# Kernel tuning notes

Measured on AMD Instinct MI355X. Metric: run time of the kernel, lower is better.

The kernel has to match this reference:

```python
import jax, jax.numpy as jnp
import numpy as np

E = 8          # num_configs
C = 256        # embed_dim
DIN = 4 * C    # embed_dim * (1 + 3 stat terms for max_order=2)
LN_EPS = 1e-5


def setup_inputs() -> dict:
    key = jax.random.key(0)
    ks = jax.random.split(key, 8)
    B, T = 4, 8192
    x = jax.random.normal(ks[0], (B, T, C), dtype=jnp.float32)
    mask = jax.random.randint(ks[1], (B, T), 0, 2, dtype=jnp.int32)
    ln_w = jnp.ones((C,), jnp.float32)
    ln_b = jnp.zeros((C,), jnp.float32)
    W1 = jax.random.normal(ks[2], (E, DIN, C), jnp.float32) / np.sqrt(DIN).astype(np.float32)
    b1 = jnp.zeros((E, C), jnp.float32)
    W2 = jax.random.normal(ks[3], (E, C, C), jnp.float32) / np.sqrt(C).astype(np.float32)
    b2 = jnp.zeros((E, C), jnp.float32)
    We = jax.random.normal(ks[4], (E, C), jnp.float32) / np.sqrt(C).astype(np.float32)
    be = jnp.zeros((E,), jnp.float32)
    log_beta = jnp.zeros((1,), jnp.float32)
    config_prior = jnp.zeros((E,), jnp.float32)
    return dict(x=x, mask=mask, ln_w=ln_w, ln_b=ln_b, W1=W1, b1=b1, W2=W2, b2=b2,
                We=We, be=be, log_beta=log_beta, config_prior=config_prior)


def _layernorm(x, w, b):
    mu = x.mean(axis=-1, keepdims=True)
    var = ((x - mu) ** 2).mean(axis=-1, keepdims=True)
    return (x - mu) * jax.lax.rsqrt(var + LN_EPS) * w + b


def reference(x, mask, ln_w, ln_b, W1, b1, W2, b2, We, be, log_beta, config_prior):
    B, T, Cd = x.shape
    m = mask.astype(bool)                         # [B,T]
    mf = m[..., None].astype(x.dtype)             # [B,T,1]

    h = _layernorm(x, ln_w, ln_b)                 # [B,T,C]

    # masked high-order statistics over T (max_order=2: mean, std, var)
    n = jnp.maximum(mf.sum(axis=1, keepdims=True), 1.0)          # [B,1,1]
    mean = (h * mf).sum(axis=1, keepdims=True) / n               # [B,1,C]
    var_b = (((h - mean) ** 2) * mf).sum(axis=1, keepdims=True) / n
    can = (n > 1.0).astype(x.dtype)
    corr = n / jnp.maximum(n - 1.0, 1e-9)
    var_u = var_b * corr * can + var_b * (1.0 - can)
    std_u = jnp.maximum(jnp.sqrt(var_u), 1e-9)

    bshape = (B, T, Cd)
    interaction = jnp.concatenate([
        x,
        jnp.broadcast_to(mean, bshape),
        jnp.broadcast_to(std_u, bshape),
        jnp.broadcast_to(var_u, bshape),
    ], axis=-1)                                                  # [B,T,4C]

    # ensemble of expert MLPs (batched over E)
    h1 = jax.nn.gelu(jnp.einsum('btd,edc->btec', interaction, W1) + b1, approximate=False)
    outputs = jnp.einsum('btec,ecf->btef', h1, W2) + b2          # [B,T,E,C]
    energies = jnp.einsum('btec,ec->bte', outputs, We) + be      # [B,T,E]

    # energy-weighted softmax mixture (partition function)
    beta = jnp.exp(log_beta)[0]
    neg_be = -beta * (energies + config_prior)                   # [B,T,E]
    big = jnp.finfo(x.dtype).max
    masked_nbe = jnp.where(m[..., None], neg_be, -big)
    log_Z = jax.nn.logsumexp(masked_nbe, axis=-1)                # [B,T]
    config_probs = jnp.exp(masked_nbe - log_Z[..., None]) * mf   # [B,T,E]

    out = jnp.einsum('bte,btec->btc', config_probs, outputs) * mf
    return out
```

## Files before the change

kernel.cpp:

```cpp
#include <hip/hip_runtime.h>
#include <cmath>

#define B_ 4
#define T_ 8192
#define C_ 256
#define E_ 8
#define M_ (B_*T_)

typedef __bf16 bf16x8 __attribute__((ext_vector_type(8)));
typedef float  f32x4  __attribute__((ext_vector_type(4)));

typedef const __attribute__((address_space(1))) unsigned int* gas_t;
typedef __attribute__((address_space(3))) unsigned int* las_t;

static __device__ __forceinline__ unsigned short f2bf(float f) {
    union { float fv; unsigned u; } v; v.fv = f;
    unsigned r = v.u + 0x7FFFu + ((v.u >> 16) & 1u);
    return (unsigned short)(r >> 16);
}

static __device__ __forceinline__ float fast_erf(float x) {
    float ax = fabsf(x);
    float t = __builtin_amdgcn_rcpf(1.0f + 0.3275911f * ax);
    float p = ((((1.061405429f * t - 1.453152027f) * t) + 1.421413741f) * t - 0.284496736f) * t + 0.254829592f;
    float y = 1.0f - p * t * __expf(-ax * ax);
    return copysignf(y, x);
}

static __device__ __forceinline__ float gelu_f(float x) {
    return 0.5f * x * (1.0f + fast_erf(x * 0.7071067811865476f));
}

static __device__ __forceinline__ f32x4 mfma16(bf16x8 a, bf16x8 b, f32x4 c) {
    return __builtin_amdgcn_mfma_f32_16x16x32_bf16(a, b, c, 0, 0, 0);
}

static __device__ __forceinline__ void stage_strip(const unsigned short* __restrict__ src,
                                                   unsigned short* base, int lane) {
#pragma unroll
    for (int j = 0; j < 8; j++) {
        int s = (j << 6) + lane;
        int col = s >> 3;
        int ks = (s & 7) ^ (col & 7);
        const unsigned short* gp = src + (col << 8) + (ks << 3);
        __builtin_amdgcn_global_load_lds((gas_t)(const void*)gp,
                                         (las_t)(void*)(base + (j << 9)), 16, 0, 0);
    }
}


__global__ void k_w1t(const float* __restrict__ W1, unsigned short* __restrict__ w1t) {
    __shared__ float tile[64][65];
    int e = blockIdx.x >> 4, kt = (blockIdx.x >> 2) & 3, ct = blockIdx.x & 3;
    int k0 = kt << 6, c0 = ct << 6;
    const float* src = W1 + ((size_t)e << 18) + ((size_t)k0 << 8) + c0;
    int r = threadIdx.x >> 6, col = threadIdx.x & 63;
#pragma unroll
    for (int i = 0; i < 16; i++)
        tile[r + i * 4][col] = src[(size_t)(r + i * 4) * 256 + col];
    __syncthreads();
    unsigned short* dst = w1t + (e << 16) + (c0 << 8) + k0;
#pragma unroll
    for (int i = 0; i < 16; i++)
        dst[(r + i * 4) * 256 + col] = f2bf(tile[col][r + i * 4]);
}

__global__ void k_w2t(const float* __restrict__ W2, unsigned short* __restrict__ w2t) {
    __shared__ float tile[64][65];
    int e = blockIdx.x >> 4, ct = (blockIdx.x >> 2) & 3, ft = blockIdx.x & 3;
    int c0 = ct << 6, f0 = ft << 6;
    const float* src = W2 + ((size_t)e << 16) + ((size_t)c0 << 8) + f0;
    int r = threadIdx.x >> 6, col = threadIdx.x & 63;
#pragma unroll
    for (int i = 0; i < 16; i++)
        tile[r + i * 4][col] = src[(size_t)(r + i * 4) * 256 + col];
    __syncthreads();
    unsigned short* dst = w2t + (e << 16) + (f0 << 8) + c0;
#pragma unroll
    for (int i = 0; i < 16; i++)
        dst[(r + i * 4) * 256 + col] = f2bf(tile[col][r + i * 4]);
}

__global__ void k_v2(const float* __restrict__ W2, const float* __restrict__ We,
                     const float* __restrict__ b2, const float* __restrict__ be,
                     const float* __restrict__ log_beta, const float* __restrict__ prior,
                     float* __restrict__ v2, float* __restrict__ bc2, float* __restrict__ bbeta) {
    __shared__ float sm[4];
    int e = blockIdx.x >> 8, c = blockIdx.x & 255, f = threadIdx.x;
    float wef = We[(e << 8) + f];
    float v = W2[((((e << 8) + c) << 8)) + f] * wef;
#pragma unroll
    for (int m = 32; m >= 1; m >>= 1) v += __shfl_xor(v, m);
    if ((f & 63) == 0) sm[f >> 6] = v;
    __syncthreads();
    if (f == 0) v2[(e << 8) + c] = sm[0] + sm[1] + sm[2] + sm[3];
    if (c == 0) {
        __syncthreads();
        float u = b2[(e << 8) + f] * wef;
#pragma unroll
        for (int m = 32; m >= 1; m >>= 1) u += __shfl_xor(u, m);
        if ((f & 63) == 0) sm[f >> 6] = u;
        __syncthreads();
        if (f == 0) {
            float beta = __expf(log_beta[0]);
            float c2e = sm[0] + sm[1] + sm[2] + sm[3] + be[e];
            bc2[e] = -beta * (c2e + prior[e]);
            if (e == 0) bbeta[0] = beta;
        }
    }
}

__global__ void k_stats(const float* __restrict__ x, const int* __restrict__ mask,
                        const float* __restrict__ lnw, const float* __restrict__ lnb,
                        float* __restrict__ S1, float* __restrict__ S2, float* __restrict__ ncnt,
                        unsigned short* __restrict__ xb) {
    int b = blockIdx.x >> 6;
    int chunk = blockIdx.x & 63;
    int wid = threadIdx.x >> 6, lane = threadIdx.x & 63;
    int c0 = lane << 2;
    float4 w4 = *reinterpret_cast<const float4*>(lnw + c0);
    float4 b4 = *reinterpret_cast<const float4*>(lnb + c0);
    float a1[4] = {0,0,0,0}, a2[4] = {0,0,0,0};
    int cnt = 0;
    int tbase = chunk * 128;
    for (int r = wid; r < 128; r += 4) {
        int row = b * T_ + tbase + r;
        float4 xv = *reinterpret_cast<const float4*>(x + (size_t)row * C_ + c0);
        ushort4 o;
        o.x = f2bf(xv.x); o.y = f2bf(xv.y); o.z = f2bf(xv.z); o.w = f2bf(xv.w);
        *reinterpret_cast<ushort4*>(xb + (size_t)row * C_ + c0) = o;
        float s1 = xv.x + xv.y + xv.z + xv.w;
        float s2 = xv.x*xv.x + xv.y*xv.y + xv.z*xv.z + xv.w*xv.w;
#pragma unroll
        for (int m = 1; m < 64; m <<= 1) { s1 += __shfl_xor(s1, m); s2 += __shfl_xor(s2, m); }
        if (mask[row]) {
            float mu = s1 * (1.f / C_);
            float var = s2 * (1.f / C_) - mu * mu;
            float rs = rsqrtf(var + 1e-5f);
            float hv;
            hv = (xv.x - mu) * rs * w4.x + b4.x; a1[0] += hv; a2[0] += hv * hv;
            hv = (xv.y - mu) * rs * w4.y + b4.y; a1[1] += hv; a2[1] += hv * hv;
            hv = (xv.z - mu) * rs * w4.z + b4.z; a1[2] += hv; a2[2] += hv * hv;
            hv = (xv.w - mu) * rs * w4.w + b4.w; a1[3] += hv; a2[3] += hv * hv;
            cnt++;
        }
    }
    __shared__ float red[4][256];
    __shared__ int rc[4];
#pragma unroll
    for (int j = 0; j < 4; j++) red[wid][c0 + j] = a1[j];
    if (lane == 0) rc[wid] = cnt;
    __syncthreads();
    int ch = threadIdx.x;
    float s = red[0][ch] + red[1][ch] + red[2][ch] + red[3][ch];
    atomicAdd(&S1[(b << 8) + ch], s);
    if (threadIdx.x == 0) atomicAdd(&ncnt[b], (float)(rc[0] + rc[1] + rc[2] + rc[3]));
    __syncthreads();
#pragma unroll
    for (int j = 0; j < 4; j++) red[wid][c0 + j] = a2[j];
    __syncthreads();
    s = red[0][ch] + red[1][ch] + red[2][ch] + red[3][ch];
    atomicAdd(&S2[(b << 8) + ch], s);
}

__global__ void k_stats_fin(const float* __restrict__ S1, const float* __restrict__ S2,
                            const float* __restrict__ ncnt, float* __restrict__ stats) {
    int b = blockIdx.x, c = threadIdx.x;
    float n = fmaxf(ncnt[b], 1.f);
    float mean = S1[(b << 8) + c] / n;
    float var_b = fmaxf(S2[(b << 8) + c] / n - mean * mean, 0.f);
    float var_u = (n > 1.f) ? (var_b * (n / fmaxf(n - 1.f, 1e-9f))) : var_b;
    float std_u = fmaxf(sqrtf(var_u), 1e-9f);
    stats[b * 768 + 0 * 256 + c] = mean;
    stats[b * 768 + 1 * 256 + c] = std_u;
    stats[b * 768 + 2 * 256 + c] = var_u;
}

__global__ void k_bias(const float* __restrict__ W1, const float* __restrict__ b1,
                       const float* __restrict__ stats, float* __restrict__ bias) {
    int b = blockIdx.x >> 3, e = blockIdx.x & 7, c = threadIdx.x;
    __shared__ float sm[768];
    for (int i = threadIdx.x; i < 768; i += 256) sm[i] = stats[b * 768 + i];
    __syncthreads();
    const float* w = W1 + (size_t)e * 1024 * 256;
    float acc = b1[(e << 8) + c];
#pragma unroll 4
    for (int j = 0; j < 256; j++) {
        acc += sm[j]       * w[(256 + j) * 256 + c];
        acc += sm[256 + j] * w[(512 + j) * 256 + c];
        acc += sm[512 + j] * w[(768 + j) * 256 + c];
    }
    bias[((b << 3) + e) * 256 + c] = acc;
}


__global__ __launch_bounds__(256, 2) void k_fused(
    const unsigned short* __restrict__ xb, const unsigned short* __restrict__ w1t,
    const unsigned short* __restrict__ w2t, const float* __restrict__ bias,
    const float* __restrict__ v2, const float* __restrict__ bc2,
    const float* __restrict__ bbeta, const int* __restrict__ mask,
    const float* __restrict__ b2, float* __restrict__ out) {
    __shared__ unsigned short sbuf[4][2][4096];
    __shared__ unsigned short h1s[32][256];
    float* scr = reinterpret_cast<float*>(&h1s[0][0]);

    int row0 = blockIdx.x << 5;
    int b = row0 >> 13;
    int tid = threadIdx.x;
    int w = tid >> 6, lane = tid & 63;
    int nco = w << 6;
    int rlo = lane & 15, khi = lane >> 4;
    unsigned short* buf0 = &sbuf[w][0][0];
    unsigned short* buf1 = &sbuf[w][1][0];

    float beta = bbeta[0];

    bf16x8 areg[2][8];
#pragma unroll
    for (int mt = 0; mt < 2; mt++)
#pragma unroll
        for (int kk = 0; kk < 8; kk++)
            areg[mt][kk] = __builtin_nontemporal_load(reinterpret_cast<const bf16x8*>(
                xb + (size_t)(row0 + (mt << 4) + rlo) * C_ + (kk << 5) + (khi << 3)));

    f32x4 acc2[2][4];
#pragma unroll
    for (int mt = 0; mt < 2; mt++)
#pragma unroll
        for (int nt = 0; nt < 4; nt++)
#pragma unroll
            for (int i = 0; i < 4; i++) acc2[mt][nt][i] = 0.f;
    float m_run[2][4], s_run[2][4];
#pragma unroll
    for (int mt = 0; mt < 2; mt++)
#pragma unroll
        for (int i = 0; i < 4; i++) { m_run[mt][i] = -3.0e38f; s_run[mt][i] = 0.f; }

    asm volatile("" ::: "memory");
    stage_strip(w1t + (w << 14), buf0, lane);

    for (int e = 0; e < E_; e++) {
        float bv[4], v2v[4], b2v[4];
#pragma unroll
        for (int nt = 0; nt < 4; nt++) {
            bv[nt]  = bias[(((b << 3) + e) << 8) + nco + (nt << 4) + rlo];
            v2v[nt] = v2[(e << 8) + nco + (nt << 4) + rlo];
            b2v[nt] = b2[(e << 8) + nco + (nt << 4) + rlo];
        }
        float bce = bc2[e];
        asm volatile("" ::: "memory");

        f32x4 acc1[2][4];
#pragma unroll
        for (int mt = 0; mt < 2; mt++)
#pragma unroll
            for (int nt = 0; nt < 4; nt++)
#pragma unroll
                for (int i = 0; i < 4; i++) acc1[mt][nt][i] = 0.f;

#pragma unroll
        for (int g = 0; g < 4; g++) {
            int p = (e << 3) + g;
            int np = p + 1;
            if (np < 64) {
                int q = np & 7;
                const unsigned short* nsrc = ((q & 4) ? w2t : w1t)
                    + ((np >> 3) << 16) + (w << 14) + ((q & 3) << 6);
                stage_strip(nsrc, (np & 1) ? buf1 : buf0, lane);
                asm volatile("s_waitcnt vmcnt(8)" ::: "memory");
            } else {
                asm volatile("s_waitcnt vmcnt(0)" ::: "memory");
            }
            const unsigned short* bs = (p & 1) ? buf1 : buf0;
            __builtin_amdgcn_s_setprio(1);
#pragma unroll
            for (int kk2 = 0; kk2 < 2; kk2++) {
                int ks = (kk2 << 2) + khi;
#pragma unroll
                for (int nt = 0; nt < 4; nt++) {
                    int col = (nt << 4) + rlo;
                    int slot = (col << 3) + (ks ^ (col & 7));
                    bf16x8 bf = *reinterpret_cast<const bf16x8*>(bs + (slot << 3));
                    acc1[0][nt] = mfma16(areg[0][(g << 1) + kk2], bf, acc1[0][nt]);
                    acc1[1][nt] = mfma16(areg[1][(g << 1) + kk2], bf, acc1[1][nt]);
                }
            }
            __builtin_amdgcn_s_setprio(0);
        }

        float rr[2][4], uu[2][4];
        {
            float epr[2][4];
#pragma unroll
            for (int mt = 0; mt < 2; mt++)
#pragma unroll
                for (int i = 0; i < 4; i++) {
                    float s = 0.f;
#pragma unroll
                    for (int nt = 0; nt < 4; nt++) {
                        float gl = gelu_f(acc1[mt][nt][i] + bv[nt]);
                        acc1[mt][nt][i] = gl;
                        s += gl * v2v[nt];
                    }
                    epr[mt][i] = s;
                }
#pragma unroll
            for (int m = 1; m < 16; m <<= 1)
#pragma unroll
                for (int mt = 0; mt < 2; mt++)
#pragma unroll
                    for (int i = 0; i < 4; i++) epr[mt][i] += __shfl_xor(epr[mt][i], m);
            if (rlo == 0) {
#pragma unroll
                for (int mt = 0; mt < 2; mt++)
#pragma unroll
                    for (int i = 0; i < 4; i++)
                        scr[(w << 5) + (mt << 4) + (khi << 2) + i] = epr[mt][i];
            }
            asm volatile("s_waitcnt lgkmcnt(0)" ::: "memory");
            __builtin_amdgcn_s_barrier();
#pragma unroll
            for (int mt = 0; mt < 2; mt++)
#pragma unroll
                for (int i = 0; i < 4; i++) {
                    int ridx = (mt << 4) + (khi << 2) + i;
                    float en = scr[ridx] + scr[32 + ridx] + scr[64 + ridx] + scr[96 + ridx];
                    float nb = -beta * en + bce;
                    float mn = fmaxf(m_run[mt][i], nb);
                    rr[mt][i] = __expf(m_run[mt][i] - mn);
                    uu[mt][i] = __expf(nb - mn);
                    s_run[mt][i] = s_run[mt][i] * rr[mt][i] + uu[mt][i];
                    m_run[mt][i] = mn;
                }
            __builtin_amdgcn_s_barrier();
#pragma unroll
            for (int mt = 0; mt < 2; mt++)
#pragma unroll
                for (int i = 0; i < 4; i++) {
                    int rowl = (mt << 4) + (khi << 2) + i;
#pragma unroll
                    for (int nt = 0; nt < 4; nt++) {
                        int col = nco + (nt << 4) + rlo;
                        int byteoff = ((rowl << 9) + (col << 1)) ^ ((rowl & 7) << 4);
                        *reinterpret_cast<unsigned short*>(reinterpret_cast<char*>(h1s) + byteoff)
                            = f2bf(acc1[mt][nt][i] * uu[mt][i]);
                    }
                }
#pragma unroll
            for (int mt = 0; mt < 2; mt++)
#pragma unroll
                for (int nt = 0; nt < 4; nt++)
#pragma unroll
                    for (int i = 0; i < 4; i++) acc1[mt][nt][i] = uu[mt][i] * b2v[nt];
        }
        asm volatile("s_waitcnt lgkmcnt(0)" ::: "memory");
        __builtin_amdgcn_s_barrier();

#pragma unroll
        for (int g = 0; g < 4; g++) {
            int p = (e << 3) + 4 + g;
            int np = p + 1;
            if (np < 64) {
                int q = np & 7;
                const unsigned short* nsrc = ((q & 4) ? w2t : w1t)
                    + ((np >> 3) << 16) + (w << 14) + ((q & 3) << 6);
                stage_strip(nsrc, (np & 1) ? buf1 : buf0, lane);
                asm volatile("s_waitcnt vmcnt(8)" ::: "memory");
            } else {
                asm volatile("s_waitcnt vmcnt(0)" ::: "memory");
            }
            const unsigned short* bs = (p & 1) ? buf1 : buf0;
            __builtin_amdgcn_s_setprio(1);
#pragma unroll
            for (int kk2 = 0; kk2 < 2; kk2++) {
                int ks = (kk2 << 2) + khi;
                bf16x8 a2[2];
#pragma unroll
                for (int mt = 0; mt < 2; mt++) {
                    int rowA = (mt << 4) + rlo;
                    int byteoff = ((rowA << 9) + (g << 7) + (kk2 << 6) + (khi << 4))
                                  ^ ((rowA & 7) << 4);
                    a2[mt] = *reinterpret_cast<const bf16x8*>(
                        reinterpret_cast<const char*>(h1s) + byteoff);
                }
#pragma unroll
                for (int nt = 0; nt < 4; nt++) {
                    int col = (nt << 4) + rlo;
                    int slot = (col << 3) + (ks ^ (col & 7));
                    bf16x8 bf = *reinterpret_cast<const bf16x8*>(bs + (slot << 3));
                    acc1[0][nt] = mfma16(a2[0], bf, acc1[0][nt]);
                    acc1[1][nt] = mfma16(a2[1], bf, acc1[1][nt]);
                }
            }
            __builtin_amdgcn_s_setprio(0);
        }
#pragma unroll
        for (int mt = 0; mt < 2; mt++)
#pragma unroll
            for (int nt = 0; nt < 4; nt++)
#pragma unroll
                for (int i = 0; i < 4; i++)
                    acc2[mt][nt][i] = acc2[mt][nt][i] * rr[mt][i] + acc1[mt][nt][i];
    }
#pragma unroll
    for (int mt = 0; mt < 2; mt++)
#pragma unroll
        for (int i = 0; i < 4; i++) {
            int rowl = (mt << 4) + (khi << 2) + i;
            int mreg = mask[row0 + rowl];
            float si = mreg ? (1.0f / s_run[mt][i]) : 0.f;
            float* orow = out + (size_t)(row0 + rowl) * C_;
#pragma unroll
            for (int nt = 0; nt < 4; nt++)
                __builtin_nontemporal_store(acc2[mt][nt][i] * si,
                                            orow + nco + (nt << 4) + rlo);
        }
}


extern "C" void kernel_launch(void* const* d_in, const int* in_sizes, int n_in,
                              void* d_out, int out_size, void* d_ws, size_t ws_size,
                              hipStream_t stream) {
    (void)in_sizes; (void)n_in; (void)out_size; (void)ws_size;
    const float* x        = (const float*)d_in[0];
    const int*   mask     = (const int*)d_in[1];
    const float* lnw      = (const float*)d_in[2];
    const float* lnb      = (const float*)d_in[3];
    const float* W1       = (const float*)d_in[4];
    const float* b1       = (const float*)d_in[5];
    const float* W2       = (const float*)d_in[6];
    const float* b2       = (const float*)d_in[7];
    const float* We       = (const float*)d_in[8];
    const float* be       = (const float*)d_in[9];
    const float* log_beta = (const float*)d_in[10];
    const float* prior    = (const float*)d_in[11];
    float* out = (float*)d_out;
    char* ws = (char*)d_ws;

    constexpr size_t OFF_XB    = 0;
    constexpr size_t OFF_W1T   = 16777216;
    constexpr size_t OFF_W2T   = 17825792;
    constexpr size_t OFF_V2    = 18874368;
    constexpr size_t OFF_BC2   = 18882560;
    constexpr size_t OFF_S1    = 18882592;
    constexpr size_t OFF_S2    = 18886688;
    constexpr size_t OFF_N     = 18890784;
    constexpr size_t OFF_STATS = 18890800;
    constexpr size_t OFF_BIAS  = 18903088;
    constexpr size_t OFF_BB    = 18935856;

    unsigned short* xb  = (unsigned short*)(ws + OFF_XB);
    unsigned short* w1t = (unsigned short*)(ws + OFF_W1T);
    unsigned short* w2t = (unsigned short*)(ws + OFF_W2T);
    float* v2    = (float*)(ws + OFF_V2);
    float* bc2   = (float*)(ws + OFF_BC2);
    float* S1    = (float*)(ws + OFF_S1);
    float* S2    = (float*)(ws + OFF_S2);
    float* ncnt  = (float*)(ws + OFF_N);
    float* stats = (float*)(ws + OFF_STATS);
    float* bias  = (float*)(ws + OFF_BIAS);
    float* bbeta = (float*)(ws + OFF_BB);

    hipMemsetAsync(ws + OFF_S1, 0, 4096 + 4096 + 16, stream);

    k_w1t<<<128, 256, 0, stream>>>(W1, w1t);
    k_w2t<<<128, 256, 0, stream>>>(W2, w2t);
    k_v2<<<2048, 256, 0, stream>>>(W2, We, b2, be, log_beta, prior, v2, bc2, bbeta);
    k_stats<<<256, 256, 0, stream>>>(x, mask, lnw, lnb, S1, S2, ncnt, xb);
    k_stats_fin<<<4, 256, 0, stream>>>(S1, S2, ncnt, stats);
    k_bias<<<32, 256, 0, stream>>>(W1, b1, stats, bias);
    k_fused<<<1024, 256, 0, stream>>>(xb, w1t, w2t, bias, v2, bc2, bbeta, mask, b2, out);
}
```

Measured before the change: 237.4 us.

## Stage x tile in LDS per expert instead of holding it in registers

Removes the 16 bf16x8 register-resident copies of the x rows (about 64 VGPRs) and instead reloads the 32-row x tile into a swizzled LDS buffer with global_load_lds at the start of each expert iteration. The buffer is shared with the h1 tile, and the energy scratch area moves into the weight staging buffer. This frees registers and LDS to raise occupancy. In exchange it adds repeated global loads of x per expert, extra barriers, an LDS read for the A operand in GEMM1, and a full vmcnt(0) drain each iteration.

```diff
diff --git a/kernel.cpp b/kernel.cpp
--- a/kernel.cpp
+++ b/kernel.cpp
@@ -201,8 +201,8 @@
     const float* __restrict__ bbeta, const int* __restrict__ mask,
     const float* __restrict__ b2, float* __restrict__ out) {
     __shared__ unsigned short sbuf[4][2][4096];
-    __shared__ unsigned short h1s[32][256];
-    float* scr = reinterpret_cast<float*>(&h1s[0][0]);
+    __shared__ unsigned short atile[8192];
+    float* scr = reinterpret_cast<float*>(&sbuf[0][1][0]);
 
     int row0 = blockIdx.x << 5;
     int b = row0 >> 13;
@@ -215,14 +215,6 @@
 
     float beta = bbeta[0];
 
-    bf16x8 areg[2][8];
-#pragma unroll
-    for (int mt = 0; mt < 2; mt++)
-#pragma unroll
-        for (int kk = 0; kk < 8; kk++)
-            areg[mt][kk] = __builtin_nontemporal_load(reinterpret_cast<const bf16x8*>(
-                xb + (size_t)(row0 + (mt << 4) + rlo) * C_ + (kk << 5) + (khi << 3)));
-
     f32x4 acc2[2][4];
 #pragma unroll
     for (int mt = 0; mt < 2; mt++)
@@ -240,6 +232,16 @@
     stage_strip(w1t + (w << 14), buf0, lane);
 
     for (int e = 0; e < E_; e++) {
+        if (e > 0) __builtin_amdgcn_s_barrier();
+#pragma unroll
+        for (int i = 0; i < 4; i++) {
+            int u = (i << 8) + (w << 6) + lane;
+            int r = u >> 5;
+            int uc = (u & 24) | ((u & 7) ^ (r & 7));
+            const unsigned short* gp = xb + (size_t)(row0 + r) * C_ + (uc << 3);
+            __builtin_amdgcn_global_load_lds((gas_t)(const void*)gp,
+                (las_t)(void*)(atile + (((i << 8) + (w << 6)) << 3)), 16, 0, 0);
+        }
         float bv[4], v2v[4], b2v[4];
 #pragma unroll
         for (int nt = 0; nt < 4; nt++) {
@@ -248,7 +250,8 @@
             b2v[nt] = b2[(e << 8) + nco + (nt << 4) + rlo];
         }
         float bce = bc2[e];
-        asm volatile("" ::: "memory");
+        asm volatile("s_waitcnt vmcnt(0) lgkmcnt(0)" ::: "memory");
+        __builtin_amdgcn_s_barrier();
 
         f32x4 acc1[2][4];
 #pragma unroll
@@ -262,27 +265,34 @@
         for (int g = 0; g < 4; g++) {
             int p = (e << 3) + g;
             int np = p + 1;
-            if (np < 64) {
+            {
                 int q = np & 7;
                 const unsigned short* nsrc = ((q & 4) ? w2t : w1t)
                     + ((np >> 3) << 16) + (w << 14) + ((q & 3) << 6);
                 stage_strip(nsrc, (np & 1) ? buf1 : buf0, lane);
                 asm volatile("s_waitcnt vmcnt(8)" ::: "memory");
-            } else {
-                asm volatile("s_waitcnt vmcnt(0)" ::: "memory");
             }
             const unsigned short* bs = (p & 1) ? buf1 : buf0;
             __builtin_amdgcn_s_setprio(1);
 #pragma unroll
             for (int kk2 = 0; kk2 < 2; kk2++) {
                 int ks = (kk2 << 2) + khi;
+                bf16x8 a[2];
+#pragma unroll
+                for (int mt = 0; mt < 2; mt++) {
+                    int rowA = (mt << 4) + rlo;
+                    int byteoff = ((rowA << 9) + (g << 7) + (kk2 << 6) + (khi << 4))
+                                  ^ ((rowA & 7) << 4);
+                    a[mt] = *reinterpret_cast<const bf16x8*>(
+                        reinterpret_cast<const char*>(atile) + byteoff);
+                }
 #pragma unroll
                 for (int nt = 0; nt < 4; nt++) {
                     int col = (nt << 4) + rlo;
                     int slot = (col << 3) + (ks ^ (col & 7));
                     bf16x8 bf = *reinterpret_cast<const bf16x8*>(bs + (slot << 3));
-                    acc1[0][nt] = mfma16(areg[0][(g << 1) + kk2], bf, acc1[0][nt]);
-                    acc1[1][nt] = mfma16(areg[1][(g << 1) + kk2], bf, acc1[1][nt]);
+                    acc1[0][nt] = mfma16(a[0], bf, acc1[0][nt]);
+                    acc1[1][nt] = mfma16(a[1], bf, acc1[1][nt]);
                 }
             }
             __builtin_amdgcn_s_setprio(0);
@@ -310,6 +320,7 @@
                 for (int mt = 0; mt < 2; mt++)
 #pragma unroll
                     for (int i = 0; i < 4; i++) epr[mt][i] += __shfl_xor(epr[mt][i], m);
+            __builtin_amdgcn_s_barrier();
             if (rlo == 0) {
 #pragma unroll
                 for (int mt = 0; mt < 2; mt++)
@@ -332,7 +343,6 @@
                     s_run[mt][i] = s_run[mt][i] * rr[mt][i] + uu[mt][i];
                     m_run[mt][i] = mn;
                 }
-            __builtin_amdgcn_s_barrier();
 #pragma unroll
             for (int mt = 0; mt < 2; mt++)
 #pragma unroll
@@ -342,7 +352,7 @@
                     for (int nt = 0; nt < 4; nt++) {
                         int col = nco + (nt << 4) + rlo;
                         int byteoff = ((rowl << 9) + (col << 1)) ^ ((rowl & 7) << 4);
-                        *reinterpret_cast<unsigned short*>(reinterpret_cast<char*>(h1s) + byteoff)
+                        *reinterpret_cast<unsigned short*>(reinterpret_cast<char*>(atile) + byteoff)
                             = f2bf(acc1[mt][nt][i] * uu[mt][i]);
                     }
                 }
@@ -381,7 +391,7 @@
                     int byteoff = ((rowA << 9) + (g << 7) + (kk2 << 6) + (khi << 4))
                                   ^ ((rowA & 7) << 4);
                     a2[mt] = *reinterpret_cast<const bf16x8*>(
-                        reinterpret_cast<const char*>(h1s) + byteoff);
+                        reinterpret_cast<const char*>(atile) + byteoff);
                 }
 #pragma unroll
                 for (int nt = 0; nt < 4; nt++) {
```

After: 209.2 us, median of 2. 11.9% less time.
